# Kernel optimization log

Measured on AMD Instinct MI355X. Metric: run time of the kernel, lower is better.

Reference implementation:

```python
import jax, jax.numpy as jnp
import numpy as np

T, B, C = 1024, 16, 1024
H, K, PAD_L = 16, 7, 3  # num_heads, kernel_size, padding_l
OUT = 1024


def setup_inputs() -> dict:
    key = jax.random.key(0)
    ks = jax.random.split(key, 8)
    s_in = 1.0 / np.sqrt(C)
    return {
        "x": jax.random.normal(ks[0], (T, B, C), dtype=jnp.float32),
        "W1": jax.random.normal(ks[1], (C, C), dtype=jnp.float32) * s_in,
        "b1": jnp.zeros((C,), dtype=jnp.float32),
        "Wq": jax.random.normal(ks[2], (C, H * K), dtype=jnp.float32) * s_in,
        "bq": jnp.zeros((H * K,), dtype=jnp.float32),
        "conv_bias": jax.random.normal(ks[3], (C,), dtype=jnp.float32) * 0.02,
        "W2": jax.random.normal(ks[4], (C, OUT), dtype=jnp.float32) * s_in,
        "b2": jnp.zeros((OUT,), dtype=jnp.float32),
    }


def reference(x, W1, b1, Wq, bq, conv_bias, W2, b2):
    # linear1 (glu=False -> no activation)
    h = x @ W1 + b1                       # [T, B, C]
    Tn, Bn, Cn = h.shape
    R = Cn // H                           # channels per head
    # dynamic filter prediction from query (= h), softmax over K taps
    w = (h @ Wq + bq).reshape(Tn, Bn, H, K)
    w = jax.nn.softmax(w, axis=-1)        # [T, B, H, K]
    # unfold1d: pad PAD_L left, K-1-PAD_L right along time, gather K-windows
    hp = jnp.pad(h, ((PAD_L, K - 1 - PAD_L), (0, 0), (0, 0)))
    win = jnp.stack([hp[k:k + Tn] for k in range(K)], axis=-1)  # [T, B, C, K]
    win = win.reshape(Tn, Bn, H, R, K)
    out = jnp.einsum('tbhrk,tbhk->tbhr', win, w).reshape(Tn, Bn, Cn)
    out = out + conv_bias                 # [T, B, C]
    return out @ W2 + b2                  # [T, B, OUT]
```

## Files before the change

### kernel.cpp

```cpp
#include <hip/hip_runtime.h>
#include <math.h>

#define T_DIM 1024
#define B_DIM 16
#define C_DIM 1024
#define H_DIM 16
#define K_TAPS 7
#define PAD_LEFT 3
#define OUT_DIM 1024
#define M_DIM (T_DIM * B_DIM)
#define HK 112
#define HKP 128
#define KD 1024

typedef __attribute__((ext_vector_type(8))) short bf16x8;
typedef __attribute__((ext_vector_type(4))) float f32x4;

__device__ __forceinline__ ushort f2bf(float f) {
    union { float f; unsigned u; } v; v.f = f;
    unsigned u = v.u;
    u += 0x7fffu + ((u >> 16) & 1u);
    return (ushort)(u >> 16);
}
__device__ __forceinline__ float bf2f(ushort h) {
    union { unsigned u; float f; } v; v.u = ((unsigned)h) << 16;
    return v.f;
}

__global__ __launch_bounds__(256) void prep(const float* __restrict__ x,
                                            ushort* __restrict__ xb,
                                            const float* __restrict__ W1s,
                                            const float* __restrict__ Wqs,
                                            const float* __restrict__ W2s,
                                            ushort* __restrict__ W1t,
                                            ushort* __restrict__ Wqt,
                                            ushort* __restrict__ W2t) {
    __shared__ float tile[32][33];
    const int bx = blockIdx.x;
    if (bx < 8192) {
        int i = bx * 256 + threadIdx.x;
        const float4* p = (const float4*)x;
        float4 a = p[2 * i], b = p[2 * i + 1];
        uint4 o;
        o.x = (unsigned)f2bf(a.x) | ((unsigned)f2bf(a.y) << 16);
        o.y = (unsigned)f2bf(a.z) | ((unsigned)f2bf(a.w) << 16);
        o.z = (unsigned)f2bf(b.x) | ((unsigned)f2bf(b.y) << 16);
        o.w = (unsigned)f2bf(b.z) | ((unsigned)f2bf(b.w) << 16);
        ((uint4*)xb)[i] = o;
        return;
    }
    int tb  = bx - 8192;
    int nbx = tb % 68;
    int k0  = (tb / 68) * 32;
    const float* W; ushort* Wt; int N, Npad, nb;
    if (nbx < 32)      { W = W1s; Wt = W1t; N = 1024; Npad = 1024; nb = nbx; }
    else if (nbx < 36) { W = Wqs; Wt = Wqt; N = 112;  Npad = 128;  nb = nbx - 32; }
    else               { W = W2s; Wt = W2t; N = 1024; Npad = 1024; nb = nbx - 36; }
    int n0 = nb * 32;
    int tx = threadIdx.x & 31, ty = threadIdx.x >> 5;
#pragma unroll
    for (int j = 0; j < 4; ++j) {
        int k = k0 + ty * 4 + j;
        int n = n0 + tx;
        tile[ty * 4 + j][tx] = (n < N) ? W[(size_t)k * N + n] : 0.f;
    }
    __syncthreads();
#pragma unroll
    for (int j = 0; j < 4; ++j) {
        int n = n0 + ty * 4 + j;
        if (n < Npad)
            Wt[(size_t)n * KD + k0 + tx] = f2bf(tile[tx][ty * 4 + j]);
    }
}

#define MPHASE(SLOT, STAGE_STMT, VM_STMT)                                     \
    {                                                                         \
        bf16x8 b[4], a_[8];                                                   \
        _Pragma("unroll")                                                     \
        for (int n = 0; n < 4; ++n)                                           \
            b[n] = *(const bf16x8*)(Bbase + (SLOT)*8192 + bOff + n*512);      \
        _Pragma("unroll")                                                     \
        for (int m = 0; m < 8; ++m)                                           \
            a_[m] = *(const bf16x8*)(Abase + (SLOT)*8192 + aOff +             \
                                     (m >> 2)*2048 + (m & 3)*512);            \
        STAGE_STMT;                                                           \
        VM_STMT;                                                              \
        __builtin_amdgcn_s_barrier();                                         \
        asm volatile("s_waitcnt lgkmcnt(0)" ::: "memory");                    \
        __builtin_amdgcn_sched_barrier(0);                                    \
        __builtin_amdgcn_s_setprio(1);                                        \
        _Pragma("unroll")                                                     \
        for (int m = 0; m < 8; ++m)                                           \
            _Pragma("unroll")                                                 \
            for (int n = 0; n < 4; ++n)                                       \
                acc[m][n] = __builtin_amdgcn_mfma_f32_16x16x32_bf16(          \
                    a_[m], b[n], acc[m][n], 0, 0, 0);                         \
        __builtin_amdgcn_s_setprio(0);                                        \
        __builtin_amdgcn_s_barrier();                                         \
        __builtin_amdgcn_sched_barrier(0);                                    \
    }

template <bool OUT_BF16>
__global__ __launch_bounds__(512, 1) void gemm8p(
    const ushort* __restrict__ A, const ushort* __restrict__ Bt,
    const float* __restrict__ bias, void* __restrict__ Cp, int ldc) {
    __shared__ ushort Lds[8 * 8192];

    const int tid  = threadIdx.x;
    const int lane = tid & 63;
    const int wid  = tid >> 6;
    const int wr = wid >> 2;
    const int wc = wid & 3;
    const int fr = lane & 15;
    const int fq = lane >> 4;

    const int orig = blockIdx.x;
    const int nid  = (orig & 7) * 32 + (orig >> 3);
    const int bm = (nid >> 2) * 256;
    const int bn = (nid & 3) * 256;

    const int srow = tid >> 2;
    const int scol = ((tid & 3) ^ ((tid >> 3) & 3)) * 8;
    const size_t sA = (size_t)(bm + srow) * KD + scol;
    const size_t sB = (size_t)(bn + srow) * KD + scol;
    const int sdst = wid * 64 * 8;

    const int slotSw = (fq ^ ((fr >> 1) & 3)) * 8;
    const int aOff = (wr * 128 + fr) * 32 + slotSw;
    const int bOff = (wc * 64 + fr) * 32 + slotSw;
    const ushort* Abase = &Lds[0];
    const ushort* Bbase = &Lds[4 * 8192];

    f32x4 acc[8][4];
#pragma unroll
    for (int m = 0; m < 8; ++m)
#pragma unroll
        for (int n = 0; n < 4; ++n) acc[m][n] = (f32x4){0.f, 0.f, 0.f, 0.f};

    auto stageA = [&](int slot, int koff) {
#pragma unroll
        for (int i = 0; i < 2; ++i)
            __builtin_amdgcn_global_load_lds(
                (const __attribute__((address_space(1))) void*)(A + sA + koff + (size_t)i * 128 * KD),
                (__attribute__((address_space(3))) void*)(&Lds[slot * 8192 + i * 4096 + sdst]),
                16, 0, 0);
    };
    auto stageB = [&](int slot, int koff) {
#pragma unroll
        for (int i = 0; i < 2; ++i)
            __builtin_amdgcn_global_load_lds(
                (const __attribute__((address_space(1))) void*)(Bt + sB + koff + (size_t)i * 128 * KD),
                (__attribute__((address_space(3))) void*)(&Lds[(4 + slot) * 8192 + i * 4096 + sdst]),
                16, 0, 0);
    };

    stageA(0, 0);   stageB(0, 0);
    stageA(1, 32);  stageB(1, 32);
    stageA(2, 64);  stageB(2, 64);
    stageA(3, 96);  stageB(3, 96);
    asm volatile("s_waitcnt vmcnt(12)" ::: "memory");
    __builtin_amdgcn_sched_barrier(0);
    __builtin_amdgcn_s_barrier();
    __builtin_amdgcn_sched_barrier(0);

#pragma unroll 1
    for (int j = 0; j < 8; ++j) {
        const int e = 2 * j;

        MPHASE(0,
               { if (j >= 1) { stageA(3, (e + 1) * 64 + 32);
                               stageB(3, (e + 1) * 64 + 32); } },
               { asm volatile("s_waitcnt vmcnt(8)" ::: "memory");
                 __builtin_amdgcn_sched_barrier(0); })
        MPHASE(1,
               { if (j < 7) { stageA(0, (e + 2) * 64);
                              stageB(0, (e + 2) * 64); } },
               { if (j == 7) { asm volatile("s_waitcnt vmcnt(4)" ::: "memory"); }
                 else        { asm volatile("s_waitcnt vmcnt(8)" ::: "memory"); }
                 __builtin_amdgcn_sched_barrier(0); })
        MPHASE(2,
               { if (j < 7) { stageA(1, (e + 2) * 64 + 32);
                              stageB(1, (e + 2) * 64 + 32); } },
               { if (j == 7) { asm volatile("s_waitcnt vmcnt(0)" ::: "memory"); }
                 else        { asm volatile("s_waitcnt vmcnt(8)" ::: "memory"); }
                 __builtin_amdgcn_sched_barrier(0); })
        MPHASE(3,
               { if (j < 7) { stageA(2, (e + 3) * 64);
                              stageB(2, (e + 3) * 64); } },
               { if (j < 7) { asm volatile("s_waitcnt vmcnt(8)" ::: "memory");
                              __builtin_amdgcn_sched_barrier(0); } })
    }

#pragma unroll
    for (int n = 0; n < 4; ++n) {
        int col = bn + wc * 64 + n * 16 + fr;
        float bv = bias[col];
#pragma unroll
        for (int m = 0; m < 8; ++m) {
#pragma unroll
            for (int r = 0; r < 4; ++r) {
                int row = bm + wr * 128 + m * 16 + fq * 4 + r;
                float v = acc[m][n][r] + bv;
                if (OUT_BF16)
                    ((ushort*)Cp)[(size_t)row * ldc + col] = f2bf(v);
                else
                    ((float*)Cp)[(size_t)row * ldc + col] = v;
            }
        }
    }
}

__global__ __launch_bounds__(256) void gemm_small(const ushort* __restrict__ A,
                                                  const ushort* __restrict__ Bt,
                                                  const float* __restrict__ bias,
                                                  float* __restrict__ Cp) {
    __shared__ ushort Als[64 * 32];
    __shared__ ushort Bls[128 * 32];
    const int tid  = threadIdx.x;
    const int lane = tid & 63;
    const int wid  = tid >> 6;
    const int wr = wid >> 1, wc = wid & 1;
    const int bm = blockIdx.y * 64;
    const int fq = lane >> 4, fr = lane & 15;

    f32x4 acc[2][4];
#pragma unroll
    for (int m = 0; m < 2; ++m)
#pragma unroll
        for (int n = 0; n < 4; ++n) acc[m][n] = (f32x4){0.f, 0.f, 0.f, 0.f};

    const int rA = tid >> 2, oA = (tid & 3) * 8;
    for (int k0 = 0; k0 < KD; k0 += 32) {
        __builtin_amdgcn_global_load_lds(
            (const __attribute__((address_space(1))) void*)&A[(size_t)(bm + rA) * KD + k0 + oA],
            (__attribute__((address_space(3))) void*)&Als[wid * 64 * 8], 16, 0, 0);
#pragma unroll
        for (int i = 0; i < 2; ++i) {
            int c = i * 256 + tid;
            __builtin_amdgcn_global_load_lds(
                (const __attribute__((address_space(1))) void*)&Bt[(size_t)(c >> 2) * KD + k0 + (c & 3) * 8],
                (__attribute__((address_space(3))) void*)&Bls[(i * 256 + wid * 64) * 8], 16, 0, 0);
        }
        __syncthreads();

        bf16x8 af[2], bfr[4];
#pragma unroll
        for (int m = 0; m < 2; ++m)
            af[m] = *(const bf16x8*)&Als[(wr * 32 + m * 16 + fr) * 32 + fq * 8];
#pragma unroll
        for (int n = 0; n < 4; ++n)
            bfr[n] = *(const bf16x8*)&Bls[(wc * 64 + n * 16 + fr) * 32 + fq * 8];
#pragma unroll
        for (int m = 0; m < 2; ++m)
#pragma unroll
            for (int n = 0; n < 4; ++n)
                acc[m][n] = __builtin_amdgcn_mfma_f32_16x16x32_bf16(
                    af[m], bfr[n], acc[m][n], 0, 0, 0);
        __syncthreads();
    }

#pragma unroll
    for (int m = 0; m < 2; ++m) {
#pragma unroll
        for (int n = 0; n < 4; ++n) {
            int col = wc * 64 + n * 16 + fr;
            if (col >= HK) continue;
            float bv = bias[col];
#pragma unroll
            for (int r = 0; r < 4; ++r) {
                int row = bm + wr * 32 + m * 16 + fq * 4 + r;
                Cp[(size_t)row * HK + col] = acc[m][n][r] + bv;
            }
        }
    }
}

__global__ __launch_bounds__(256) void dynconv2(const ushort* __restrict__ h,
                                                const float* __restrict__ q,
                                                const float* __restrict__ cbias,
                                                ushort* __restrict__ out) {
    __shared__ ushort hw[22][1024];
    __shared__ float wsm[16][HK];
    const int tid = threadIdx.x;
    const int b  = blockIdx.x & 15;
    const int t0 = (blockIdx.x >> 4) << 4;

    for (int i = tid; i < 22 * 128; i += 256) {
        int wrow = i >> 7;
        int c8   = (i & 127) * 8;
        int tt   = t0 + wrow - PAD_LEFT;
        uint4 v = make_uint4(0, 0, 0, 0);
        if (tt >= 0 && tt < T_DIM)
            v = *(const uint4*)&h[((size_t)tt * B_DIM + b) * C_DIM + c8];
        *(uint4*)&hw[wrow][c8] = v;
    }
    {
        int tl = tid >> 4, hh = tid & 15;
        int m = (t0 + tl) * B_DIM + b;
        const float* p = &q[(size_t)m * HK + hh * K_TAPS];
        float mx = p[0];
#pragma unroll
        for (int k = 1; k < K_TAPS; ++k) mx = fmaxf(mx, p[k]);
        float e[K_TAPS], s = 0.f;
#pragma unroll
        for (int k = 0; k < K_TAPS; ++k) { e[k] = __expf(p[k] - mx); s += e[k]; }
        float inv = 1.f / s;
#pragma unroll
        for (int k = 0; k < K_TAPS; ++k) wsm[tl][hh * K_TAPS + k] = e[k] * inv;
    }
    __syncthreads();

    const int c  = tid * 4;
    const int hh = c >> 6;
    float4 bias = *(const float4*)&cbias[c];

    for (int tl = 0; tl < 16; ++tl) {
        float a0 = bias.x, a1 = bias.y, a2 = bias.z, a3 = bias.w;
#pragma unroll
        for (int k = 0; k < K_TAPS; ++k) {
            ushort4 hv = *(const ushort4*)&hw[tl + k][c];
            float wk = wsm[tl][hh * K_TAPS + k];
            a0 = fmaf(bf2f(hv.x), wk, a0);
            a1 = fmaf(bf2f(hv.y), wk, a1);
            a2 = fmaf(bf2f(hv.z), wk, a2);
            a3 = fmaf(bf2f(hv.w), wk, a3);
        }
        ushort4 o;
        o.x = f2bf(a0); o.y = f2bf(a1); o.z = f2bf(a2); o.w = f2bf(a3);
        *(ushort4*)&out[((size_t)(t0 + tl) * B_DIM + b) * C_DIM + c] = o;
    }
}

extern "C" void kernel_launch(void* const* d_in, const int* in_sizes, int n_in,
                              void* d_out, int out_size, void* d_ws,
                              size_t ws_size, hipStream_t stream) {
    const float* x     = (const float*)d_in[0];
    const float* W1    = (const float*)d_in[1];
    const float* b1    = (const float*)d_in[2];
    const float* Wq    = (const float*)d_in[3];
    const float* bq    = (const float*)d_in[4];
    const float* cbias = (const float*)d_in[5];
    const float* W2    = (const float*)d_in[6];
    const float* b2    = (const float*)d_in[7];
    float* out = (float*)d_out;

    ushort* xb    = (ushort*)d_ws;
    ushort* hb    = xb    + (size_t)M_DIM * C_DIM;
    ushort* convb = hb    + (size_t)M_DIM * C_DIM;
    ushort* W1t   = convb + (size_t)M_DIM * C_DIM;
    ushort* W2t   = W1t   + (size_t)C_DIM * C_DIM;
    ushort* Wqt   = W2t   + (size_t)C_DIM * OUT_DIM;
    float*  q     = (float*)(Wqt + (size_t)HKP * C_DIM);

    prep<<<dim3(8192 + 68 * 32), dim3(256), 0, stream>>>(
        x, xb, W1, Wq, W2, W1t, Wqt, W2t);

    gemm8p<true><<<dim3(256), dim3(512), 0, stream>>>(xb, W1t, b1, hb, C_DIM);

    gemm_small<<<dim3(1, M_DIM / 64), dim3(256), 0, stream>>>(hb, Wqt, bq, q);

    dynconv2<<<dim3(B_DIM * T_DIM / 16), dim3(256), 0, stream>>>(
        hb, q, cbias, convb);

    gemm8p<false><<<dim3(256), dim3(512), 0, stream>>>(convb, W2t, b2, out,
                                                       OUT_DIM);
}
```

Baseline: 147.3 us.

## Use 256x128 GEMM tiles with register double-buffered LDS reads overlapping MFMA

Both large GEMMs now use 256x128 tiles instead of 256x256, launching 512 workgroups instead of 256, with a 4x2 wave layout and 4x4 accumulators per wave. The main loop keeps two register fragment sets so LDS reads for the next k-slice are issued while MFMAs on the current slice run, with one barrier per phase instead of two. The intent is more parallelism across CUs and hiding LDS read latency behind compute. The cost is lower per-tile operand reuse, more global traffic for A, and fewer MFMAs per phase to cover sync overhead.

```diff
diff --git a/kernel.cpp b/kernel.cpp
--- a/kernel.cpp
+++ b/kernel.cpp
@@ -73,133 +73,132 @@
     }
 }
 
-#define MPHASE(SLOT, STAGE_STMT, VM_STMT)                                     \
-    {                                                                         \
-        bf16x8 b[4], a_[8];                                                   \
+#define READF(FA, FB, SLOT)                                                   \
+    _Pragma("unroll")                                                         \
+    for (int m = 0; m < 4; ++m)                                               \
+        FA[m] = *(const bf16x8*)(Ab + (SLOT)*8192 + aOff + m*512);            \
+    _Pragma("unroll")                                                         \
+    for (int n = 0; n < 4; ++n)                                               \
+        FB[n] = *(const bf16x8*)(Bb + (SLOT)*4096 + bOff + n*512);
+
+#define MFMAB(FA, FB)                                                         \
+    __builtin_amdgcn_s_setprio(1);                                            \
+    _Pragma("unroll")                                                         \
+    for (int m = 0; m < 4; ++m)                                               \
         _Pragma("unroll")                                                     \
         for (int n = 0; n < 4; ++n)                                           \
-            b[n] = *(const bf16x8*)(Bbase + (SLOT)*8192 + bOff + n*512);      \
-        _Pragma("unroll")                                                     \
-        for (int m = 0; m < 8; ++m)                                           \
-            a_[m] = *(const bf16x8*)(Abase + (SLOT)*8192 + aOff +             \
-                                     (m >> 2)*2048 + (m & 3)*512);            \
-        STAGE_STMT;                                                           \
-        VM_STMT;                                                              \
-        __builtin_amdgcn_s_barrier();                                         \
+            acc[m][n] = __builtin_amdgcn_mfma_f32_16x16x32_bf16(              \
+                FA[m], FB[n], acc[m][n], 0, 0, 0);                            \
+    __builtin_amdgcn_s_setprio(0);
+
+#define VM3 asm volatile("s_waitcnt vmcnt(3)" ::: "memory")
+#define VM0 asm volatile("s_waitcnt vmcnt(0)" ::: "memory")
+
+#define OLPHASE(CA, CB, NA, NB, RSLOT, DO_STAGE, SSLOT, SKSUB, VMS)           \
+    {                                                                         \
+        if (DO_STAGE) stage(SSLOT, SKSUB);                                    \
+        READF(NA, NB, RSLOT)                                                  \
+        __builtin_amdgcn_sched_barrier(0);                                    \
+        MFMAB(CA, CB)                                                         \
         asm volatile("s_waitcnt lgkmcnt(0)" ::: "memory");                    \
+        VMS;                                                                  \
         __builtin_amdgcn_sched_barrier(0);                                    \
-        __builtin_amdgcn_s_setprio(1);                                        \
-        _Pragma("unroll")                                                     \
-        for (int m = 0; m < 8; ++m)                                           \
-            _Pragma("unroll")                                                 \
-            for (int n = 0; n < 4; ++n)                                       \
-                acc[m][n] = __builtin_amdgcn_mfma_f32_16x16x32_bf16(          \
-                    a_[m], b[n], acc[m][n], 0, 0, 0);                         \
-        __builtin_amdgcn_s_setprio(0);                                        \
         __builtin_amdgcn_s_barrier();                                         \
         __builtin_amdgcn_sched_barrier(0);                                    \
     }
 
 template <bool OUT_BF16>
-__global__ __launch_bounds__(512, 1) void gemm8p(
+__global__ __launch_bounds__(512, 1) void gemm_ol(
     const ushort* __restrict__ A, const ushort* __restrict__ Bt,
     const float* __restrict__ bias, void* __restrict__ Cp, int ldc) {
-    __shared__ ushort Lds[8 * 8192];
+    __shared__ ushort Lds[4 * 8192 + 4 * 4096];
 
     const int tid  = threadIdx.x;
     const int lane = tid & 63;
     const int wid  = tid >> 6;
-    const int wr = wid >> 2;
-    const int wc = wid & 3;
+    const int wr = wid >> 1;
+    const int wc = wid & 1;
     const int fr = lane & 15;
     const int fq = lane >> 4;
 
     const int orig = blockIdx.x;
-    const int nid  = (orig & 7) * 32 + (orig >> 3);
-    const int bm = (nid >> 2) * 256;
-    const int bn = (nid & 3) * 256;
-
-    const int srow = tid >> 2;
-    const int scol = ((tid & 3) ^ ((tid >> 3) & 3)) * 8;
-    const size_t sA = (size_t)(bm + srow) * KD + scol;
-    const size_t sB = (size_t)(bn + srow) * KD + scol;
-    const int sdst = wid * 64 * 8;
+    const int nid  = (orig & 7) * 64 + (orig >> 3);
+    const int bm = (nid >> 3) * 256;
+    const int bn = (nid & 7) * 128;
+
+    const int rA    = tid >> 2;
+    const int colSw = ((tid & 3) ^ ((tid >> 3) & 3)) * 8;
+    const size_t srcA0 = (size_t)(bm + rA) * KD + colSw;
+    const size_t srcB0 = (size_t)(bn + rA) * KD + colSw;
 
     const int slotSw = (fq ^ ((fr >> 1) & 3)) * 8;
-    const int aOff = (wr * 128 + fr) * 32 + slotSw;
+    const int aOff = (wr * 64 + fr) * 32 + slotSw;
     const int bOff = (wc * 64 + fr) * 32 + slotSw;
-    const ushort* Abase = &Lds[0];
-    const ushort* Bbase = &Lds[4 * 8192];
-
-    f32x4 acc[8][4];
-#pragma unroll
-    for (int m = 0; m < 8; ++m)
+    const ushort* Ab = &Lds[0];
+    const ushort* Bb = &Lds[4 * 8192];
+
+    f32x4 acc[4][4];
+#pragma unroll
+    for (int m = 0; m < 4; ++m)
 #pragma unroll
         for (int n = 0; n < 4; ++n) acc[m][n] = (f32x4){0.f, 0.f, 0.f, 0.f};
 
-    auto stageA = [&](int slot, int koff) {
+    auto stage = [&](int slot, int ksub) {
+        const ushort* Ap = A + srcA0 + ksub * 32;
+        const ushort* Bp = Bt + srcB0 + ksub * 32;
 #pragma unroll
         for (int i = 0; i < 2; ++i)
             __builtin_amdgcn_global_load_lds(
-                (const __attribute__((address_space(1))) void*)(A + sA + koff + (size_t)i * 128 * KD),
-                (__attribute__((address_space(3))) void*)(&Lds[slot * 8192 + i * 4096 + sdst]),
+                (const __attribute__((address_space(1))) void*)(Ap + (size_t)i * 128 * KD),
+                (__attribute__((address_space(3))) void*)(&Lds[slot * 8192 + i * 4096 + wid * 512]),
                 16, 0, 0);
+        __builtin_amdgcn_global_load_lds(
+            (const __attribute__((address_space(1))) void*)Bp,
+            (__attribute__((address_space(3))) void*)(&Lds[4 * 8192 + slot * 4096 + wid * 512]),
+            16, 0, 0);
     };
-    auto stageB = [&](int slot, int koff) {
-#pragma unroll
-        for (int i = 0; i < 2; ++i)
-            __builtin_amdgcn_global_load_lds(
-                (const __attribute__((address_space(1))) void*)(Bt + sB + koff + (size_t)i * 128 * KD),
-                (__attribute__((address_space(3))) void*)(&Lds[(4 + slot) * 8192 + i * 4096 + sdst]),
-                16, 0, 0);
-    };
-
-    stageA(0, 0);   stageB(0, 0);
-    stageA(1, 32);  stageB(1, 32);
-    stageA(2, 64);  stageB(2, 64);
-    stageA(3, 96);  stageB(3, 96);
-    asm volatile("s_waitcnt vmcnt(12)" ::: "memory");
+
+    bf16x8 f0a[4], f0b[4], f1a[4], f1b[4];
+
+    stage(0, 0);
+    stage(1, 1);
+    stage(2, 2);
+    VM3;
     __builtin_amdgcn_sched_barrier(0);
     __builtin_amdgcn_s_barrier();
     __builtin_amdgcn_sched_barrier(0);
+    READF(f0a, f0b, 0)
+    asm volatile("s_waitcnt lgkmcnt(0)" ::: "memory");
+    __builtin_amdgcn_sched_barrier(0);
 
 #pragma unroll 1
-    for (int j = 0; j < 8; ++j) {
-        const int e = 2 * j;
-
-        MPHASE(0,
-               { if (j >= 1) { stageA(3, (e + 1) * 64 + 32);
-                               stageB(3, (e + 1) * 64 + 32); } },
-               { asm volatile("s_waitcnt vmcnt(8)" ::: "memory");
-                 __builtin_amdgcn_sched_barrier(0); })
-        MPHASE(1,
-               { if (j < 7) { stageA(0, (e + 2) * 64);
-                              stageB(0, (e + 2) * 64); } },
-               { if (j == 7) { asm volatile("s_waitcnt vmcnt(4)" ::: "memory"); }
-                 else        { asm volatile("s_waitcnt vmcnt(8)" ::: "memory"); }
-                 __builtin_amdgcn_sched_barrier(0); })
-        MPHASE(2,
-               { if (j < 7) { stageA(1, (e + 2) * 64 + 32);
-                              stageB(1, (e + 2) * 64 + 32); } },
-               { if (j == 7) { asm volatile("s_waitcnt vmcnt(0)" ::: "memory"); }
-                 else        { asm volatile("s_waitcnt vmcnt(8)" ::: "memory"); }
-                 __builtin_amdgcn_sched_barrier(0); })
-        MPHASE(3,
-               { if (j < 7) { stageA(2, (e + 3) * 64);
-                              stageB(2, (e + 3) * 64); } },
-               { if (j < 7) { asm volatile("s_waitcnt vmcnt(8)" ::: "memory");
-                              __builtin_amdgcn_sched_barrier(0); } })
-    }
+    for (int j = 0; j < 7; ++j) {
+        const int k4 = 4 * j;
+        OLPHASE(f0a, f0b, f1a, f1b, 1, true, 3, k4 + 3, VM3)
+        OLPHASE(f1a, f1b, f0a, f0b, 2, true, 0, k4 + 4, VM3)
+        OLPHASE(f0a, f0b, f1a, f1b, 3, true, 1, k4 + 5, VM3)
+        OLPHASE(f1a, f1b, f0a, f0b, 0, true, 2, k4 + 6, VM3)
+    }
+    OLPHASE(f0a, f0b, f1a, f1b, 1, true, 3, 31, VM3)
+    OLPHASE(f1a, f1b, f0a, f0b, 2, false, 0, 0, VM0)
+    {
+        READF(f1a, f1b, 3)
+        __builtin_amdgcn_sched_barrier(0);
+        MFMAB(f0a, f0b)
+        asm volatile("s_waitcnt lgkmcnt(0)" ::: "memory");
+        __builtin_amdgcn_sched_barrier(0);
+    }
+    MFMAB(f1a, f1b)
 
 #pragma unroll
     for (int n = 0; n < 4; ++n) {
         int col = bn + wc * 64 + n * 16 + fr;
         float bv = bias[col];
 #pragma unroll
-        for (int m = 0; m < 8; ++m) {
+        for (int m = 0; m < 4; ++m) {
 #pragma unroll
             for (int r = 0; r < 4; ++r) {
-                int row = bm + wr * 128 + m * 16 + fq * 4 + r;
+                int row = bm + wr * 64 + m * 16 + fq * 4 + r;
                 float v = acc[m][n][r] + bv;
                 if (OUT_BF16)
                     ((ushort*)Cp)[(size_t)row * ldc + col] = f2bf(v);
@@ -355,13 +354,13 @@
     prep<<<dim3(8192 + 68 * 32), dim3(256), 0, stream>>>(
         x, xb, W1, Wq, W2, W1t, Wqt, W2t);
 
-    gemm8p<true><<<dim3(256), dim3(512), 0, stream>>>(xb, W1t, b1, hb, C_DIM);
+    gemm_ol<true><<<dim3(512), dim3(512), 0, stream>>>(xb, W1t, b1, hb, C_DIM);
 
     gemm_small<<<dim3(1, M_DIM / 64), dim3(256), 0, stream>>>(hb, Wqt, bq, q);
 
     dynconv2<<<dim3(B_DIM * T_DIM / 16), dim3(256), 0, stream>>>(
         hb, q, cbias, convb);
 
-    gemm8p<false><<<dim3(256), dim3(512), 0, stream>>>(convb, W2t, b2, out,
-                                                       OUT_DIM);
-}
+    gemm_ol<false><<<dim3(512), dim3(512), 0, stream>>>(convb, W2t, b2, out,
+                                                        OUT_DIM);
+}
```

After: 151.8 us. +3.0%, slower.
